# Performance work log

Hardware: AMD Instinct MI355X
Metric: run time of the kernel (lower is better)

Reference implementation:

```python
import jax, jax.numpy as jnp
import numpy as np

D_MODEL = 1024
D_KV = 64
N_HEADS = 16
INNER = N_HEADS * D_KV
EPS = 1e-6


def setup_inputs() -> dict:
    key = jax.random.key(0)
    ks = jax.random.split(key, 8)
    B, SQ, SKV = 2, 2048, 4096
    hidden_states = jax.random.normal(ks[0], (B, SQ, D_MODEL), dtype=jnp.float32)
    key_value_states = jax.random.normal(ks[1], (B, SKV, D_MODEL), dtype=jnp.float32)
    attention_mask = jnp.zeros((B, 1, 1, SKV), dtype=jnp.float32)
    # nn.Linear(in, out, bias=False): y = x @ W.T; store W as [in, out] here
    s = 0.02
    Wq = jax.random.normal(ks[2], (D_MODEL, INNER), dtype=jnp.float32) * s
    Wk = jax.random.normal(ks[3], (D_MODEL, INNER), dtype=jnp.float32) * s
    Wv = jax.random.normal(ks[4], (D_MODEL, INNER), dtype=jnp.float32) * s
    Wo = jax.random.normal(ks[5], (INNER, D_MODEL), dtype=jnp.float32) * s
    ln_weight = jnp.ones((D_MODEL,), dtype=jnp.float32)
    return {
        "hidden_states": hidden_states,
        "key_value_states": key_value_states,
        "attention_mask": attention_mask,
        "ln_weight": ln_weight,
        "Wq": Wq,
        "Wk": Wk,
        "Wv": Wv,
        "Wo": Wo,
    }


def _t5_rmsnorm(x, w, eps=EPS):
    # no mean subtraction, variance in fp32
    var = jnp.mean(jnp.square(x.astype(jnp.float32)), axis=-1, keepdims=True)
    return w * (x * jax.lax.rsqrt(var + eps)).astype(x.dtype)


def reference(hidden_states, key_value_states, attention_mask, ln_weight, Wq, Wk, Wv, Wo):
    B, SQ, _ = hidden_states.shape
    SKV = key_value_states.shape[1]
    normed = _t5_rmsnorm(hidden_states, ln_weight)

    # projections -> [B, H, S, Dk]
    q = (normed @ Wq).reshape(B, SQ, N_HEADS, D_KV).transpose(0, 2, 1, 3)
    k = (key_value_states @ Wk).reshape(B, SKV, N_HEADS, D_KV).transpose(0, 2, 1, 3)
    v = (key_value_states @ Wv).reshape(B, SKV, N_HEADS, D_KV).transpose(0, 2, 1, 3)

    # T5: NO 1/sqrt(d) scaling
    scores = jnp.einsum("bhqd,bhkd->bhqk", q, k) + attention_mask
    attn = jax.nn.softmax(scores.astype(jnp.float32), axis=-1).astype(scores.dtype)
    ctx = jnp.einsum("bhqk,bhkd->bhqd", attn, v)
    ctx = ctx.transpose(0, 2, 1, 3).reshape(B, SQ, INNER)
    attn_out = ctx @ Wo
    return hidden_states + attn_out
```

## Files before the change

kernel.cpp:

```cpp
#include <hip/hip_runtime.h>

typedef unsigned short u16;
typedef unsigned int u32;
typedef __attribute__((ext_vector_type(4))) float f32x4;
typedef __attribute__((ext_vector_type(8))) short short8;
typedef __attribute__((ext_vector_type(4))) short short4v;

#define BB   2
#define SQL  2048
#define SKVL 4096
#define DM   1024
#define NH   16
#define DK   64
#define L2E  1.44269504f

#if __has_builtin(__builtin_amdgcn_exp2f)
#define EXP2(x) __builtin_amdgcn_exp2f(x)
#else
#define EXP2(x) exp2f(x)
#endif

#define MFMA32(a, b, c) __builtin_amdgcn_mfma_f32_16x16x32_bf16(a, b, c, 0, 0, 0)

__device__ __forceinline__ u16 f2bf(float f) {
  union { float f; unsigned u; } v; v.f = f;
  unsigned r = v.u + 0x7fff + ((v.u >> 16) & 1);
  return (u16)(r >> 16);
}

__device__ __forceinline__ short4v pack4(float p0, float p1, float p2, float p3) {
  union { float f; u32 u; } a, b, c, d;
  a.f = p0; b.f = p1; c.f = p2; d.f = p3;
  union { uint2 v; short4v s; } r;
  r.v.x = __builtin_amdgcn_perm(b.u + 0x8000u, a.u + 0x8000u, 0x07060302);
  r.v.y = __builtin_amdgcn_perm(d.u + 0x8000u, c.u + 0x8000u, 0x07060302);
  return r.s;
}

__device__ __forceinline__ void gload16(const void* g, void* lds) {
  __builtin_amdgcn_global_load_lds(
      (const __attribute__((address_space(1))) unsigned int*)g,
      (__attribute__((address_space(3))) unsigned int*)lds, 16, 0, 0);
}

__global__ void pre_kernel(const float* __restrict__ hidden, const float* __restrict__ lnw,
                           const float* __restrict__ kvs,
                           const float* __restrict__ Wq, const float* __restrict__ Wk,
                           const float* __restrict__ Wv, const float* __restrict__ Wo,
                           u16* __restrict__ normed, u16* __restrict__ kvb,
                           u16* __restrict__ Wqt, u16* __restrict__ Wkt,
                           u16* __restrict__ Wvt, u16* __restrict__ Wot) {
  __shared__ float red[4];
  __shared__ float tile[32][33];
  int bid = blockIdx.x, t = threadIdx.x;
  if (bid < 4096) {
    int row = bid;
    float4 v = ((const float4*)(hidden + (size_t)row * DM))[t];
    float ss = v.x * v.x + v.y * v.y + v.z * v.z + v.w * v.w;
#pragma unroll
    for (int m = 32; m >= 1; m >>= 1) ss += __shfl_xor(ss, m, 64);
    int lane = t & 63, wv = t >> 6;
    if (lane == 0) red[wv] = ss;
    __syncthreads();
    float total = red[0] + red[1] + red[2] + red[3];
    float scale = rsqrtf(total * (1.0f / DM) + 1e-6f);
    float4 g = ((const float4*)lnw)[t];
    ushort4 o;
    o.x = f2bf(v.x * scale * g.x);
    o.y = f2bf(v.y * scale * g.y);
    o.z = f2bf(v.z * scale * g.z);
    o.w = f2bf(v.w * scale * g.w);
    ((ushort4*)(normed + (size_t)row * DM))[t] = o;
  } else if (bid < 12288) {
    int i = (bid - 4096) * 256 + t;
    float4 v = ((const float4*)kvs)[i];
    ushort4 o;
    o.x = f2bf(v.x); o.y = f2bf(v.y); o.z = f2bf(v.z); o.w = f2bf(v.w);
    ((ushort4*)kvb)[i] = o;
  } else {
    int g = bid - 12288;
    int z = g >> 10;
    const float* W = (z == 0) ? Wq : (z == 1) ? Wk : (z == 2) ? Wv : Wo;
    u16* Wt = (z == 0) ? Wqt : (z == 1) ? Wkt : (z == 2) ? Wvt : Wot;
    int xx = g & 31, yy = (g >> 5) & 31;
    int tx = t & 31, ty = t >> 5;
    int k0 = yy * 32, n0 = xx * 32;
#pragma unroll
    for (int i = 0; i < 4; i++)
      tile[ty + i * 8][tx] = W[(size_t)(k0 + ty + i * 8) * DM + n0 + tx];
    __syncthreads();
#pragma unroll
    for (int i = 0; i < 4; i++)
      Wt[(size_t)(n0 + ty + i * 8) * DM + k0 + tx] = f2bf(tile[tx][ty + i * 8]);
  }
}

__global__ __launch_bounds__(512, 1) void proj_kernel(
    const u16* __restrict__ normed, const u16* __restrict__ kvb,
    const u16* __restrict__ Wqt, const u16* __restrict__ Wkt,
    const u16* __restrict__ Wvt,
    u16* __restrict__ Qb, u16* __restrict__ Kbf, u16* __restrict__ Vtb) {
  const int K = 1024;
  __shared__ __align__(16) u16 Al[256 * 32];
  __shared__ __align__(16) u16 B1[128 * 32];
  __shared__ __align__(16) u16 B2[128 * 32];
  int tid = threadIdx.x, lane = tid & 63, w = tid >> 6;
  int l15 = lane & 15, quad = lane >> 4;
  int wy = w >> 1, wx = w & 1;
  int bid = blockIdx.x;

  if (bid < 256) {
    int tm = (bid >> 3) * 256, tn = (bid & 7) * 128;
    f32x4 ak[4][4] = {}, av[4][4] = {};
    for (int k0 = 0; k0 < K; k0 += 32) {
      __syncthreads();
#pragma unroll
      for (int r = 0; r < 2; r++) {
        int mg = w * 2 + r;
        gload16(kvb + (size_t)(tm + mg * 16 + l15) * K + k0 + quad * 8, &Al[mg * 512]);
      }
      gload16(Wkt + (size_t)(tn + w * 16 + l15) * K + k0 + quad * 8, &B1[w * 512]);
      gload16(Wvt + (size_t)(tn + w * 16 + l15) * K + k0 + quad * 8, &B2[w * 512]);
      __syncthreads();
      short8 af[4], bk[4], bv[4];
#pragma unroll
      for (int i = 0; i < 4; i++) {
        af[i] = *(const short8*)&Al[((wy * 4 + i) * 64 + lane) * 8];
        bk[i] = *(const short8*)&B1[((wx * 4 + i) * 64 + lane) * 8];
        bv[i] = *(const short8*)&B2[((wx * 4 + i) * 64 + lane) * 8];
      }
#pragma unroll
      for (int mt = 0; mt < 4; mt++)
#pragma unroll
        for (int nt = 0; nt < 4; nt++) {
          ak[mt][nt] = MFMA32(af[mt], bk[nt], ak[mt][nt]);
          av[mt][nt] = MFMA32(af[mt], bv[nt], av[mt][nt]);
        }
    }
#pragma unroll
    for (int mt = 0; mt < 4; mt++) {
      int m0 = tm + wy * 64 + mt * 16 + quad * 4;
      int bB = m0 >> 12, skv0 = m0 & 4095;
      int t32 = skv0 >> 5, p0 = skv0 & 31;
#pragma unroll
      for (int nt = 0; nt < 4; nt++) {
        int n = tn + wx * 64 + nt * 16 + l15;
        int h = n >> 6, d0 = n & 63;
        size_t vbase = ((size_t)((bB * NH + h) * 128 + t32)) * 2048
                     + (size_t)(d0 >> 4) * 512 + (size_t)(d0 & 15) * 8;
#pragma unroll
        for (int r = 0; r < 4; r++) {
          Kbf[(size_t)(m0 + r) * 1024 + n] = f2bf(ak[mt][nt][r]);
          int p = p0 + r;
          int s = ((p >> 2) & 3) * 8 + ((p >> 4) & 1) * 4 + (p & 3);
          Vtb[vbase + (s >> 3) * 128 + (s & 7)] = f2bf(av[mt][nt][r]);
        }
      }
    }
  } else {
    int qid = bid - 256;
    int tm = (qid >> 3) * 128, tn = (qid & 7) * 128;
    f32x4 acc[2][4] = {};
    for (int k0 = 0; k0 < K; k0 += 32) {
      __syncthreads();
      gload16(normed + (size_t)(tm + w * 16 + l15) * K + k0 + quad * 8, &Al[w * 512]);
      gload16(Wqt + (size_t)(tn + w * 16 + l15) * K + k0 + quad * 8, &B1[w * 512]);
      __syncthreads();
      short8 af[2], bfr[4];
#pragma unroll
      for (int i = 0; i < 2; i++)
        af[i] = *(const short8*)&Al[((wy * 2 + i) * 64 + lane) * 8];
#pragma unroll
      for (int i = 0; i < 4; i++)
        bfr[i] = *(const short8*)&B1[((wx * 4 + i) * 64 + lane) * 8];
#pragma unroll
      for (int mt = 0; mt < 2; mt++)
#pragma unroll
        for (int nt = 0; nt < 4; nt++)
          acc[mt][nt] = MFMA32(af[mt], bfr[nt], acc[mt][nt]);
    }
#pragma unroll
    for (int mt = 0; mt < 2; mt++) {
      int m0 = tm + wy * 32 + mt * 16 + quad * 4;
#pragma unroll
      for (int nt = 0; nt < 4; nt++) {
        int n = tn + wx * 64 + nt * 16 + l15;
#pragma unroll
        for (int r = 0; r < 4; r++)
          Qb[(size_t)(m0 + r) * 1024 + n] = f2bf(acc[mt][nt][r] * L2E);
      }
    }
  }
}

__global__ __launch_bounds__(256, 2) void flash_kernel(
    const u16* __restrict__ Qp, const u16* __restrict__ Kp, const u16* __restrict__ Vtb,
    const float* __restrict__ mask, u16* __restrict__ ctx) {
  __shared__ __align__(16) char smem[65536];
  u16* Kbuf = (u16*)smem;
  u16* Vbuf = (u16*)(smem + 32768);
  float* Ox = (float*)smem;
  float* Ll = (float*)(smem + 32768);

  int tid = threadIdx.x, lane = tid & 63, w = tid >> 6;
  int l15 = lane & 15, quad = lane >> 4;
  int grp = w >> 1, wg = w & 1;

  int lid = blockIdx.y * 16 + blockIdx.x;
  int xcd = lid & 7, slot = lid >> 3;
  int bh = xcd * 4 + (slot >> 4);
  int qb = slot & 15;
  int b = bh >> 4, h = bh & 15;
  int q0 = qb * 128 + wg * 64;

  short8 qf[4][2];
#pragma unroll
  for (int mt = 0; mt < 4; mt++)
#pragma unroll
    for (int kf = 0; kf < 2; kf++)
      qf[mt][kf] = *(const short8*)(Qp + (size_t)(b * SQL + q0 + mt * 16 + l15) * DM +
                                    h * DK + kf * 32 + quad * 8);

  f32x4 of[4][4] = {};
  f32x4 la[4] = {};
  const short8 ones8 = {0x3F80, 0x3F80, 0x3F80, 0x3F80, 0x3F80, 0x3F80, 0x3F80, 0x3F80};

  const size_t vblob = (size_t)(b * NH + h) * 262144;
  const float* mrow = mask + (size_t)b * SKVL;

  auto stage = [&](int tileIdx, int buf) {
    int kv0 = tileIdx * 64;
    u16* Kd = Kbuf + (buf * 2 + grp) * 4096;
    u16* Vd = Vbuf + (buf * 2 + grp) * 4096;
#pragma unroll
    for (int r = 0; r < 4; r++) {
      int u = wg * 4 + r;
      int kt = u >> 1, kf = u & 1;
      gload16(Kp + (size_t)(b * SKVL + kv0 + kt * 16 + l15) * DM + h * DK + kf * 32 + quad * 8,
              &Kd[u * 512]);
      gload16(Vtb + vblob + (size_t)tileIdx * 4096 + u * 512 + lane * 8, &Vd[u * 512]);
    }
  };

  f32x4 mlc[4], mln[4];
  {
    int kv0 = grp * 64;
#pragma unroll
    for (int kt = 0; kt < 4; kt++)
      mlc[kt] = *(const f32x4*)(mrow + kv0 + kt * 16 + quad * 4) * L2E;
  }
  stage(grp, 0);

  union PU { short8 v8; short4v h2[2]; };

  for (int it = 0; it < 32; ++it) {
    __syncthreads();
    if (it + 1 < 32) {
      stage((it + 1) * 2 + grp, (it + 1) & 1);
      int kvn = ((it + 1) * 2 + grp) * 64;
#pragma unroll
      for (int kt = 0; kt < 4; kt++)
        mln[kt] = *(const f32x4*)(mrow + kvn + kt * 16 + quad * 4) * L2E;
    }
    const u16* Kg = Kbuf + ((it & 1) * 2 + grp) * 4096;
    const u16* Vg = Vbuf + ((it & 1) * 2 + grp) * 4096;

#pragma unroll
    for (int ktp = 0; ktp < 2; ktp++) {
      PU paf[4];
#pragma unroll
      for (int kth = 0; kth < 2; kth++) {
        int kt = ktp * 2 + kth;
        short8 k0 = *(const short8*)&Kg[((kt * 2 + 0) * 64 + lane) * 8];
        short8 k1 = *(const short8*)&Kg[((kt * 2 + 1) * 64 + lane) * 8];
#pragma unroll
        for (int mt = 0; mt < 4; mt++) {
          f32x4 st = mlc[kt];
          st = MFMA32(k0, qf[mt][0], st);
          st = MFMA32(k1, qf[mt][1], st);
          paf[mt].h2[kth] = pack4(EXP2(st[0]), EXP2(st[1]), EXP2(st[2]), EXP2(st[3]));
        }
      }
#pragma unroll
      for (int mt = 0; mt < 4; mt++)
        la[mt] = MFMA32(paf[mt].v8, ones8, la[mt]);
#pragma unroll
      for (int nt = 0; nt < 4; nt++) {
        short8 vv = *(const short8*)&Vg[ktp * 2048 + (nt * 64 + lane) * 8];
#pragma unroll
        for (int mt = 0; mt < 4; mt++)
          of[mt][nt] = MFMA32(paf[mt].v8, vv, of[mt][nt]);
      }
    }
#pragma unroll
    for (int kt = 0; kt < 4; kt++) mlc[kt] = mln[kt];
  }

  __syncthreads();
  if (grp == 1) {
#pragma unroll
    for (int mt = 0; mt < 4; mt++) {
#pragma unroll
      for (int nt = 0; nt < 4; nt++)
#pragma unroll
        for (int r = 0; r < 4; r++)
          Ox[(wg * 64 + mt * 16 + quad * 4 + r) * 64 + nt * 16 + l15] = of[mt][nt][r];
      if (l15 == 0)
#pragma unroll
        for (int r = 0; r < 4; r++) Ll[wg * 64 + mt * 16 + quad * 4 + r] = la[mt][r];
    }
  }
  __syncthreads();
  if (grp == 0) {
#pragma unroll
    for (int mt = 0; mt < 4; mt++)
#pragma unroll
      for (int r = 0; r < 4; r++) {
        int ql = wg * 64 + mt * 16 + quad * 4 + r;
        float inv = 1.0f / (la[mt][r] + Ll[ql]);
        int q = qb * 128 + ql;
#pragma unroll
        for (int nt = 0; nt < 4; nt++) {
          float ov = of[mt][nt][r] + Ox[ql * 64 + nt * 16 + l15];
          ctx[(size_t)(b * SQL + q) * DM + h * DK + nt * 16 + l15] = f2bf(ov * inv);
        }
      }
  }
}

__global__ void ogemm_kernel(const u16* __restrict__ A, const u16* __restrict__ Bt,
                             float* __restrict__ C, const float* __restrict__ resid) {
  const int K = 1024;
  __shared__ __align__(16) u16 Al[128 * 32];
  __shared__ __align__(16) u16 Bl[128 * 32];
  int tid = threadIdx.x, lane = tid & 63, w = tid >> 6;
  int l15 = lane & 15, quad = lane >> 4;
  int wy = w >> 1, wx = w & 1;
  int tm = blockIdx.x * 128, tn = blockIdx.y * 128;
  f32x4 acc[4][4] = {};

  for (int k0 = 0; k0 < K; k0 += 32) {
    __syncthreads();
#pragma unroll
    for (int r = 0; r < 2; r++) {
      int mg = w * 2 + r;
      gload16(A + (size_t)(tm + mg * 16 + l15) * K + k0 + quad * 8, &Al[mg * 512]);
      gload16(Bt + (size_t)(tn + mg * 16 + l15) * K + k0 + quad * 8, &Bl[mg * 512]);
    }
    __syncthreads();
    short8 af[4], bfr[4];
#pragma unroll
    for (int i = 0; i < 4; i++) {
      af[i] = *(const short8*)&Al[((wy * 4 + i) * 64 + lane) * 8];
      bfr[i] = *(const short8*)&Bl[((wx * 4 + i) * 64 + lane) * 8];
    }
#pragma unroll
    for (int mt = 0; mt < 4; mt++)
#pragma unroll
      for (int nt = 0; nt < 4; nt++)
        acc[mt][nt] = MFMA32(af[mt], bfr[nt], acc[mt][nt]);
  }

#pragma unroll
  for (int mt = 0; mt < 4; mt++) {
    int m0 = tm + wy * 64 + mt * 16 + quad * 4;
#pragma unroll
    for (int nt = 0; nt < 4; nt++) {
      int n = tn + wx * 64 + nt * 16 + l15;
#pragma unroll
      for (int r = 0; r < 4; r++) {
        size_t idx = (size_t)(m0 + r) * 1024 + n;
        C[idx] = resid[idx] + acc[mt][nt][r];
      }
    }
  }
}

extern "C" void kernel_launch(void* const* d_in, const int* in_sizes, int n_in,
                              void* d_out, int out_size, void* d_ws, size_t ws_size,
                              hipStream_t stream) {
  const float* hidden = (const float*)d_in[0];
  const float* kvs    = (const float*)d_in[1];
  const float* mask   = (const float*)d_in[2];
  const float* lnw    = (const float*)d_in[3];
  const float* Wq     = (const float*)d_in[4];
  const float* Wk     = (const float*)d_in[5];
  const float* Wv     = (const float*)d_in[6];
  const float* Wo     = (const float*)d_in[7];
  char* ws = (char*)d_ws;

  u16* normed = (u16*)(ws + 0);
  u16* kvb    = (u16*)(ws + 8388608);
  u16* Wqt    = (u16*)(ws + 25165824);
  u16* Wkt    = (u16*)(ws + 27262976);
  u16* Wvt    = (u16*)(ws + 29360128);
  u16* Wot    = (u16*)(ws + 31457280);
  u16* Qb     = (u16*)(ws + 33554432);
  u16* Kbf    = (u16*)(ws + 41943040);
  u16* Vtb    = (u16*)(ws + 58720256);
  u16* ctxb   = (u16*)(ws + 75497472);

  pre_kernel<<<16384, 256, 0, stream>>>(hidden, lnw, kvs, Wq, Wk, Wv, Wo,
                                        normed, kvb, Wqt, Wkt, Wvt, Wot);
  proj_kernel<<<512, 512, 0, stream>>>(normed, kvb, Wqt, Wkt, Wvt, Qb, Kbf, Vtb);
  flash_kernel<<<dim3(SQL / 128, BB * NH), 256, 0, stream>>>(Qb, Kbf, Vtb, mask, ctxb);
  ogemm_kernel<<<dim3(32, 8), 256, 0, stream>>>(ctxb, Wot, (float*)d_out, hidden);
}
```

Before: 310.7 us.

## Load V fragments directly from global and halve LDS to raise occupancy

The V tile is no longer staged through shared memory. Each wave now loads its pre-laid-out V fragments straight from global memory into registers at the start of each iteration, and only K is double-buffered in LDS. Shared memory drops to about 33KB, so launch bounds are raised to 3 blocks per CU. The mask values are also loaded per iteration instead of being prefetched one iteration ahead. The cost is that global-load latency for V and the mask now sits on the critical path of each iteration, and register pressure rises under the tighter occupancy bound.

```diff
diff --git a/kernel.cpp b/kernel.cpp
--- a/kernel.cpp
+++ b/kernel.cpp
@@ -193,12 +193,11 @@
   }
 }
 
-__global__ __launch_bounds__(256, 2) void flash_kernel(
+__global__ __launch_bounds__(256, 3) void flash_kernel(
     const u16* __restrict__ Qp, const u16* __restrict__ Kp, const u16* __restrict__ Vtb,
     const float* __restrict__ mask, u16* __restrict__ ctx) {
-  __shared__ __align__(16) char smem[65536];
+  __shared__ __align__(16) char smem[33280];
   u16* Kbuf = (u16*)smem;
-  u16* Vbuf = (u16*)(smem + 32768);
   float* Ox = (float*)smem;
   float* Ll = (float*)(smem + 32768);
 
@@ -228,42 +227,38 @@
   const size_t vblob = (size_t)(b * NH + h) * 262144;
   const float* mrow = mask + (size_t)b * SKVL;
 
-  auto stage = [&](int tileIdx, int buf) {
-    int kv0 = tileIdx * 64;
-    u16* Kd = Kbuf + (buf * 2 + grp) * 4096;
-    u16* Vd = Vbuf + (buf * 2 + grp) * 4096;
+  auto stage = [&](int it1) {
+    int kv0 = (it1 * 2 + grp) * 64;
+    u16* Kd = Kbuf + ((it1 & 1) * 2 + grp) * 4096;
 #pragma unroll
     for (int r = 0; r < 4; r++) {
       int u = wg * 4 + r;
       int kt = u >> 1, kf = u & 1;
       gload16(Kp + (size_t)(b * SKVL + kv0 + kt * 16 + l15) * DM + h * DK + kf * 32 + quad * 8,
               &Kd[u * 512]);
-      gload16(Vtb + vblob + (size_t)tileIdx * 4096 + u * 512 + lane * 8, &Vd[u * 512]);
     }
   };
 
-  f32x4 mlc[4], mln[4];
-  {
-    int kv0 = grp * 64;
+  stage(0);
+
+  union PU { short8 v8; short4v h2[2]; };
+
+  for (int it = 0; it < 32; ++it) {
+    int tk = it * 2 + grp;
+    __syncthreads();
+    f32x4 ml[4];
 #pragma unroll
     for (int kt = 0; kt < 4; kt++)
-      mlc[kt] = *(const f32x4*)(mrow + kv0 + kt * 16 + quad * 4) * L2E;
-  }
-  stage(grp, 0);
-
-  union PU { short8 v8; short4v h2[2]; };
-
-  for (int it = 0; it < 32; ++it) {
-    __syncthreads();
-    if (it + 1 < 32) {
-      stage((it + 1) * 2 + grp, (it + 1) & 1);
-      int kvn = ((it + 1) * 2 + grp) * 64;
-#pragma unroll
-      for (int kt = 0; kt < 4; kt++)
-        mln[kt] = *(const f32x4*)(mrow + kvn + kt * 16 + quad * 4) * L2E;
-    }
+      ml[kt] = *(const f32x4*)(mrow + tk * 64 + kt * 16 + quad * 4) * L2E;
+    short8 vv[2][4];
+#pragma unroll
+    for (int ktp = 0; ktp < 2; ktp++)
+#pragma unroll
+      for (int nt = 0; nt < 4; nt++)
+        vv[ktp][nt] = *(const short8*)(Vtb + vblob + (size_t)tk * 4096 +
+                                       ktp * 2048 + (nt * 64 + lane) * 8);
+    if (it + 1 < 32) stage(it + 1);
     const u16* Kg = Kbuf + ((it & 1) * 2 + grp) * 4096;
-    const u16* Vg = Vbuf + ((it & 1) * 2 + grp) * 4096;
 
 #pragma unroll
     for (int ktp = 0; ktp < 2; ktp++) {
@@ -275,7 +270,7 @@
         short8 k1 = *(const short8*)&Kg[((kt * 2 + 1) * 64 + lane) * 8];
 #pragma unroll
         for (int mt = 0; mt < 4; mt++) {
-          f32x4 st = mlc[kt];
+          f32x4 st = ml[kt];
           st = MFMA32(k0, qf[mt][0], st);
           st = MFMA32(k1, qf[mt][1], st);
           paf[mt].h2[kth] = pack4(EXP2(st[0]), EXP2(st[1]), EXP2(st[2]), EXP2(st[3]));
@@ -285,15 +280,11 @@
       for (int mt = 0; mt < 4; mt++)
         la[mt] = MFMA32(paf[mt].v8, ones8, la[mt]);
 #pragma unroll
-      for (int nt = 0; nt < 4; nt++) {
-        short8 vv = *(const short8*)&Vg[ktp * 2048 + (nt * 64 + lane) * 8];
+      for (int nt = 0; nt < 4; nt++)
 #pragma unroll
         for (int mt = 0; mt < 4; mt++)
-          of[mt][nt] = MFMA32(paf[mt].v8, vv, of[mt][nt]);
-      }
-    }
-#pragma unroll
-    for (int kt = 0; kt < 4; kt++) mlc[kt] = mln[kt];
+          of[mt][nt] = MFMA32(paf[mt].v8, vv[ktp][nt], of[mt][nt]);
+    }
   }
 
   __syncthreads();
```

Measured after the change: 472.0 us. +51.9%, slower.
